# Kernel tuning notes

Hardware: AMD Instinct MI355X
Metric: run time of the kernel (lower is better)

The kernel has to match this reference:

```python
import jax, jax.numpy as jnp
import numpy as np

N_HEADS = 16
ROPE_THETA = 10000.0


def _rope_cos_sin(T, head_dim, dtype):
    # freqs: (head_dim//2,), angles: (T, head_dim//2)
    freqs = 1.0 / ROPE_THETA ** (jnp.arange(0, head_dim, 2, dtype=jnp.float32) / head_dim)
    ang = jnp.arange(T, dtype=jnp.float32)[:, None] * freqs[None, :]
    return jnp.cos(ang).astype(dtype), jnp.sin(ang).astype(dtype)


def _apply_rope(x, cos, sin):
    # x: (B, H, T, D); cos/sin: (T, D//2)
    D = x.shape[-1]
    x1, x2 = x[..., : D // 2], x[..., D // 2 :]
    return jnp.concatenate([x1 * cos - x2 * sin, x1 * sin + x2 * cos], axis=-1)


def setup_inputs() -> dict:
    key = jax.random.key(0)
    ks = jax.random.split(key, 5)
    B, T, C = 2, 2048, 1024
    x = jax.random.normal(ks[0], (B, T, C), dtype=jnp.float32)
    w_attn = jax.random.normal(ks[1], (C, 3 * C), dtype=jnp.float32) * (C ** -0.5)
    b_attn = jax.random.normal(ks[2], (3 * C,), dtype=jnp.float32) * 0.02
    w_proj = jax.random.normal(ks[3], (C, C), dtype=jnp.float32) * (C ** -0.5)
    b_proj = jax.random.normal(ks[4], (C,), dtype=jnp.float32) * 0.02
    return {
        "x": x,
        "w_attn": w_attn,
        "b_attn": b_attn,
        "w_proj": w_proj,
        "b_proj": b_proj,
        "last_k_no_attend": 0,
        "window_size": 0,
    }


def reference(x, w_attn, b_attn, w_proj, b_proj, last_k_no_attend, window_size):
    B, T, C = x.shape
    H = N_HEADS
    D = C // H
    qkv = x @ w_attn + b_attn  # (B, T, 3C)
    q, k, v = jnp.split(qkv, 3, axis=-1)
    # (B, T, C) -> (B, H, T, D)
    to_heads = lambda t: t.reshape(B, T, H, D).transpose(0, 2, 1, 3)
    q, k, v = to_heads(q), to_heads(k), to_heads(v)
    cos, sin = _rope_cos_sin(T, D, x.dtype)
    q = _apply_rope(q, cos, sin)
    k = _apply_rope(k, cos, sin)
    scale = D ** -0.5
    attn = jnp.einsum("bhqd,bhkd->bhqk", q, k) * scale  # (B, H, T, T)
    causal = jnp.tril(jnp.ones((T, T), dtype=bool))
    attn = jnp.where(causal, attn, -jnp.inf)
    # last_k_no_attend/window_size default to 0 -> the custom-mask branch is
    # skipped (the nonzero branch in the source is ill-defined: it zeroes
    # entire rows producing NaN softmax).
    attn = jax.nn.softmax(attn, axis=-1)
    y = jnp.einsum("bhqk,bhkd->bhqd", attn, v)  # (B, H, T, D)
    y = y.transpose(0, 2, 1, 3).reshape(B, T, C)
    return y @ w_proj + b_proj
```

## Files before the change

kernel.cpp:

```cpp
#include <hip/hip_runtime.h>
#include <hip/hip_bf16.h>

typedef __bf16 bf16_t;
typedef __bf16 bf16x8 __attribute__((ext_vector_type(8)));
typedef float f32x4 __attribute__((ext_vector_type(4)));
typedef float f32x8v __attribute__((ext_vector_type(8)));

#define B_    2
#define T_    2048
#define C_    1024
#define H_    16
#define D_    64
#define M_    4096
#define NQKV_ 3072
#define PLD   72
#define NQT2  16
#define GTILE (128 * 64)
#define SLOT2 32768
#define KSB   4096
#define VTB   (64 * PLD)

static __device__ __forceinline__ float  bf2f(bf16_t x) { return (float)x; }
static __device__ __forceinline__ bf16_t f2bf(float x)  { return (bf16_t)x; }

typedef const __attribute__((address_space(1))) void gas_void;
typedef __attribute__((address_space(3))) void las_void;
static __device__ __forceinline__ void gld16(const void* g, void* l) {
  __builtin_amdgcn_global_load_lds((gas_void*)g, (las_void*)l, 16, 0, 0);
}

__global__ __launch_bounds__(256) void rope_tab_k(float2* __restrict__ tab) {
  int i = blockIdx.x * 256 + threadIdx.x;
  int tpos = i >> 5, d = i & 31;
  float fr = exp2f(-(float)d * (13.287712379549449f / 32.0f));
  float ang = (float)tpos * fr;
  tab[i] = make_float2(cosf(ang), sinf(ang));
}

__global__ __launch_bounds__(256) void f32_to_bf16_k(const float* __restrict__ in,
                                                     bf16_t* __restrict__ out) {
  const int i = (blockIdx.x * 256 + threadIdx.x) * 8;
  f32x8v v = *(const f32x8v*)(in + i);
  bf16x8 h;
#pragma unroll
  for (int j = 0; j < 8; ++j) h[j] = f2bf(v[j]);
  *(bf16x8*)(out + i) = h;
}

__global__ __launch_bounds__(256) void transpose_f32_bf16(const float* __restrict__ in,
                                                          bf16_t* __restrict__ out,
                                                          int R, int Ccols) {
  __shared__ bf16_t tile[32][33];
  int tx = threadIdx.x & 31, ty = threadIdx.x >> 5;
  int c0 = blockIdx.x * 32, r0 = blockIdx.y * 32;
#pragma unroll
  for (int j = 0; j < 4; ++j)
    tile[ty + j * 8][tx] = f2bf(in[(size_t)(r0 + ty + j * 8) * Ccols + c0 + tx]);
  __syncthreads();
#pragma unroll
  for (int j = 0; j < 4; ++j)
    out[(size_t)(c0 + ty + j * 8) * R + r0 + tx] = tile[tx][ty + j * 8];
}

__device__ __forceinline__ void gemm_core(const bf16_t* __restrict__ A,
                                          const bf16_t* __restrict__ Bt,
                                          int m0, int n0,
                                          bf16_t* sm,
                                          f32x4 acc[4][4]) {
  const int t    = threadIdx.x;
  const int lane = t & 63, w = t >> 6;
  const int wr = (w >> 1) * 64, wc = (w & 1) * 64;
  const int l15 = lane & 15, g4 = lane >> 4;

  const f32x4 z4 = {0.f, 0.f, 0.f, 0.f};
#pragma unroll
  for (int i = 0; i < 4; ++i)
#pragma unroll
    for (int j = 0; j < 4; ++j) acc[i][j] = z4;

  const int srow = w * 32 + (lane >> 3);
  const int sel8 = (lane & 7) * 8;
  const bf16_t* gA = A  + (size_t)(m0 + srow) * C_ + sel8;
  const bf16_t* gB = Bt + (size_t)(n0 + srow) * C_ + sel8;
  const int dOff = (w * 32) * 64;

#pragma unroll
  for (int j = 0; j < 4; ++j) {
    gld16(gA + (size_t)(j * 8) * C_, sm + dOff + j * 8 * 64);
    gld16(gB + (size_t)(j * 8) * C_, sm + GTILE + dOff + j * 8 * 64);
  }
  __syncthreads();

  int cur = 0;
  for (int kt = 0; kt < C_ / 64; ++kt) {
    if (kt + 1 < C_ / 64) {
      const int k0 = (kt + 1) * 64;
      bf16_t* nA = sm + (cur ^ 1) * (2 * GTILE);
      bf16_t* nB = nA + GTILE;
#pragma unroll
      for (int j = 0; j < 4; ++j) {
        gld16(gA + (size_t)(j * 8) * C_ + k0, nA + dOff + j * 8 * 64);
        gld16(gB + (size_t)(j * 8) * C_ + k0, nB + dOff + j * 8 * 64);
      }
    }
    const bf16_t* lA = sm + cur * (2 * GTILE);
    const bf16_t* lB = lA + GTILE;
#pragma unroll
    for (int ks = 0; ks < 2; ++ks) {
      bf16x8 af[4], bfv[4];
#pragma unroll
      for (int mi = 0; mi < 4; ++mi)
        af[mi] = *(const bf16x8*)&lA[(wr + mi * 16 + l15) * 64 + ks * 32 + g4 * 8];
#pragma unroll
      for (int ni = 0; ni < 4; ++ni)
        bfv[ni] = *(const bf16x8*)&lB[(wc + ni * 16 + l15) * 64 + ks * 32 + g4 * 8];
#pragma unroll
      for (int mi = 0; mi < 4; ++mi)
#pragma unroll
        for (int ni = 0; ni < 4; ++ni)
          acc[mi][ni] = __builtin_amdgcn_mfma_f32_16x16x32_bf16(af[mi], bfv[ni],
                                                                acc[mi][ni], 0, 0, 0);
    }
    __syncthreads();
    cur ^= 1;
  }
}

__global__ __launch_bounds__(512, 2) void qkv_gemm(const bf16_t* __restrict__ x,
                                                   const bf16_t* __restrict__ wT,
                                                   const float* __restrict__ bias,
                                                   const float2* __restrict__ rtab,
                                                   bf16_t* __restrict__ qo,
                                                   bf16_t* __restrict__ ko,
                                                   bf16_t* __restrict__ vo) {
  __shared__ __align__(16) bf16_t sm[2 * SLOT2];
  const int t = threadIdx.x;
  const int lane = t & 63, w = t >> 6;
  const int l15 = lane & 15, g4 = lane >> 4;
  const int wr = (w >> 1) * 32, wc = (w & 1) * 192;

  const int bid = blockIdx.x;
  const int swz = (bid & 7) * 32 + (bid >> 3);
  const int m0 = (swz & 31) * 128, n0 = (swz >> 5) * 384;

  const f32x4 z4 = {0.f, 0.f, 0.f, 0.f};
  f32x4 acc[2][12];
#pragma unroll
  for (int i = 0; i < 2; ++i)
#pragma unroll
    for (int j = 0; j < 12; ++j) acc[i][j] = z4;

  const int sr8 = lane >> 3;
  const int swc = ((lane & 7) ^ ((lane >> 3) & 7)) * 8;
  const bf16_t* gA = x  + (size_t)(m0 + w * 16 + sr8) * C_ + swc;
  const bf16_t* gB = wT + (size_t)(n0 + w * 48 + sr8) * C_ + swc;

#define QKV_STAGE(h)                                                            \
  {                                                                             \
    bf16_t* sl = sm + ((h) & 1) * SLOT2;                                        \
    const size_t kofs = (size_t)(h) * 64;                                       \
    gld16(gA + kofs,            sl + (w * 16 +  0) * 64);                       \
    gld16(gA +  8 * C_ + kofs,  sl + (w * 16 +  8) * 64);                       \
    gld16(gB + kofs,            sl + 8192 + (w * 48 +  0) * 64);                \
    gld16(gB +  8 * C_ + kofs,  sl + 8192 + (w * 48 +  8) * 64);                \
    gld16(gB + 16 * C_ + kofs,  sl + 8192 + (w * 48 + 16) * 64);                \
    gld16(gB + 24 * C_ + kofs,  sl + 8192 + (w * 48 + 24) * 64);                \
    gld16(gB + 32 * C_ + kofs,  sl + 8192 + (w * 48 + 32) * 64);                \
    gld16(gB + 40 * C_ + kofs,  sl + 8192 + (w * 48 + 40) * 64);                \
  }

  QKV_STAGE(0);

  const int csw = l15 & 7;

  for (int h = 0; h < 16; ++h) {
    asm volatile("s_waitcnt vmcnt(0)" ::: "memory");
    __builtin_amdgcn_sched_barrier(0);
    __builtin_amdgcn_s_barrier();
    __builtin_amdgcn_sched_barrier(0);
    if (h + 1 < 16) QKV_STAGE(h + 1);

    const bf16_t* sl = sm + (h & 1) * SLOT2;
#pragma unroll
    for (int ks = 0; ks < 2; ++ks) {
      bf16x8 af[2], bfv[12];
#pragma unroll
      for (int mi = 0; mi < 2; ++mi)
        af[mi] = *(const bf16x8*)&sl[(wr + mi * 16 + l15) * 64 + (((ks * 4 + g4) ^ csw) * 8)];
#pragma unroll
      for (int ni = 0; ni < 12; ++ni)
        bfv[ni] = *(const bf16x8*)&sl[8192 + (wc + ni * 16 + l15) * 64 + (((ks * 4 + g4) ^ csw) * 8)];
#pragma unroll
      for (int mi = 0; mi < 2; ++mi)
#pragma unroll
        for (int ni = 0; ni < 12; ++ni)
          acc[mi][ni] = __builtin_amdgcn_mfma_f32_16x16x32_bf16(af[mi], bfv[ni],
                                                                acc[mi][ni], 0, 0, 0);
    }
  }
#undef QKV_STAGE

  __syncthreads();
  bf16_t* stg = sm + w * 6144;

#pragma unroll
  for (int cc = 0; cc < 3; ++cc) {
    const int ngc = n0 + (w & 1) * 192 + cc * 64;
    const int sel = ngc >> 10;
    if (sel < 2) {
      const float qs = (sel == 0) ? 0.125f * 1.4426950408889634f : 1.0f;
#pragma unroll
      for (int mi = 0; mi < 2; ++mi) {
#pragma unroll
        for (int nq = 0; nq < 2; ++nq) {
          const int d1 = nq * 16 + l15;
          const float b1 = bias[ngc + d1];
          const float b2 = bias[ngc + d1 + 32];
#pragma unroll
          for (int r = 0; r < 4; ++r) {
            const int lrow = mi * 16 + g4 * 4 + r;
            const int tpos = (m0 + wr + lrow) & (T_ - 1);
            const float2 cs = rtab[tpos * 32 + d1];
            const float x1 = acc[mi][cc * 4 + nq][r]     + b1;
            const float x2 = acc[mi][cc * 4 + nq + 2][r] + b2;
            stg[lrow * 192 + cc * 64 + d1]      = f2bf((x1 * cs.x - x2 * cs.y) * qs);
            stg[lrow * 192 + cc * 64 + d1 + 32] = f2bf((x1 * cs.y + x2 * cs.x) * qs);
          }
        }
      }
    } else {
#pragma unroll
      for (int mi = 0; mi < 2; ++mi)
#pragma unroll
        for (int nq = 0; nq < 4; ++nq) {
          const int d = nq * 16 + l15;
          const float b1 = bias[ngc + d];
#pragma unroll
          for (int r = 0; r < 4; ++r)
            stg[(mi * 16 + g4 * 4 + r) * 192 + cc * 64 + d] = f2bf(acc[mi][cc * 4 + nq][r] + b1);
        }
    }
  }

  const int a  = lane >> 3;
  const int b8 = (lane & 7) * 8;
#pragma unroll
  for (int cc = 0; cc < 3; ++cc) {
    const int ngc = n0 + (w & 1) * 192 + cc * 64;
    const int sel = ngc >> 10;
    const int hh  = (ngc & 1023) >> 6;
    bf16_t* outp = (sel == 0) ? qo : (sel == 1 ? ko : vo);
#pragma unroll
    for (int pp = 0; pp < 4; ++pp) {
      const int lrow = pp * 8 + a;
      const int row  = m0 + wr + lrow;
      const int tpos = row & (T_ - 1);
      const int bb   = row >> 11;
      uint4 val = *(const uint4*)&stg[lrow * 192 + cc * 64 + b8];
      *(uint4*)(outp + ((size_t)(bb * H_ + hh) * T_ + tpos) * D_ + b8) = val;
    }
  }
}

__global__ __launch_bounds__(512) void attn_fwd(const bf16_t* __restrict__ q,
                                                const bf16_t* __restrict__ k,
                                                const bf16_t* __restrict__ v,
                                                bf16_t* __restrict__ y) {
  __shared__ __align__(16) bf16_t Ks[2 * KSB];
  __shared__ __align__(16) bf16_t Vt[2 * VTB];
  const int t = threadIdx.x;
  const int lane = t & 63, w = t >> 6;
  const int l15 = lane & 15, g4 = lane >> 4;

  const int f   = blockIdx.x;
  const int idx = f & 255;
  const int bh  = idx & 31;
  const int p   = idx >> 5;
  const int qt  = (f >> 8) ? (15 - p) : p;
  const int qb  = qt * 128;
  const size_t hb = (size_t)bh * T_ * D_;

  const int qrow = qb + w * 16 + l15;
  bf16x8 qf[2];
  qf[0] = *(const bf16x8*)(q + hb + (size_t)qrow * D_ + g4 * 8);
  qf[1] = *(const bf16x8*)(q + hb + (size_t)qrow * D_ + 32 + g4 * 8);

  const f32x4 z4 = {0.f, 0.f, 0.f, 0.f};
  f32x4 o[4];
#pragma unroll
  for (int i = 0; i < 4; ++i) o[i] = z4;
  float mx = -1e30f, L = 0.f;

  const int skk = t >> 3;
  const int sd0 = (t & 7) * 8;
  const int u   = t & 7;
  const int ksw = sd0 ^ ((skk & 7) * 8);
  const int slot = ((skk >> 5) & 1) * 32 + ((skk >> 2) & 3) * 8 + ((skk >> 4) & 1) * 4 + (skk & 3);
  const int pos  = (((slot >> 3) ^ u) << 3) | (slot & 7);
  const int rowb = qb + w * 16 + g4 * 4;

  const int ntiles = 2 * qt + 2;

  {
    uint4 kv0 = *(const uint4*)(k + hb + (size_t)skk * D_ + sd0);
    uint4 vv0 = *(const uint4*)(v + hb + (size_t)skk * D_ + sd0);
    *(uint4*)&Ks[skk * 64 + ksw] = kv0;
    const bf16_t* vb = (const bf16_t*)&vv0;
#pragma unroll
    for (int i = 0; i < 8; ++i)
      Vt[(sd0 + i) * PLD + pos] = vb[i];
  }
  __syncthreads();

  uint4 kv, vv;
  for (int it = 0; it < ntiles; ++it) {
    const int kb  = it * 64;
    const int cur = it & 1;
    const bool last = (it == ntiles - 1);

    if (it + 1 < ntiles) {
      const size_t nb = hb + (size_t)(kb + 64 + skk) * D_ + sd0;
      kv = *(const uint4*)(k + nb);
      vv = *(const uint4*)(v + nb);
    }

    if (!(last && w < 4)) {
      const bf16_t* KsC = Ks + cur * KSB;
      const bf16_t* VtC = Vt + cur * VTB;

      f32x4 s[4];
#pragma unroll
      for (int c = 0; c < 4; ++c) s[c] = z4;
#pragma unroll
      for (int ks = 0; ks < 2; ++ks)
#pragma unroll
        for (int c = 0; c < 4; ++c) {
          const int kr = c * 16 + l15;
          bf16x8 kf = *(const bf16x8*)&KsC[kr * 64 + ((ks * 32 + g4 * 8) ^ ((kr & 7) * 8))];
          s[c] = __builtin_amdgcn_mfma_f32_16x16x32_bf16(kf, qf[ks], s[c], 0, 0, 0);
        }

      if (last || (it == ntiles - 2 && w < 4)) {
#pragma unroll
        for (int c = 0; c < 4; ++c)
#pragma unroll
          for (int r = 0; r < 4; ++r)
            if (kb + c * 16 + g4 * 4 + r > qrow) s[c][r] = -1e30f;
      }

      float tm = -1e30f;
#pragma unroll
      for (int c = 0; c < 4; ++c)
#pragma unroll
        for (int r = 0; r < 4; ++r) tm = fmaxf(tm, s[c][r]);
      tm = fmaxf(tm, __shfl_xor(tm, 16));
      tm = fmaxf(tm, __shfl_xor(tm, 32));
      if (!__all(tm - mx <= 8.0f)) {
        const float mnew = fmaxf(mx, tm);
        const float sc = exp2f(mx - mnew);
        L *= sc;
        float scr[4];
#pragma unroll
        for (int r = 0; r < 4; ++r)
          scr[r] = __shfl(sc, (lane & 48) | (g4 * 4 + r));
#pragma unroll
        for (int nf = 0; nf < 4; ++nf)
#pragma unroll
          for (int r = 0; r < 4; ++r) o[nf][r] *= scr[r];
        mx = mnew;
      }
      float rs = 0.f;
#pragma unroll
      for (int c = 0; c < 4; ++c)
#pragma unroll
        for (int r = 0; r < 4; ++r) {
          s[c][r] = exp2f(s[c][r] - mx);
          rs += s[c][r];
        }
      rs += __shfl_xor(rs, 16);
      rs += __shfl_xor(rs, 32);
      L += rs;

      bf16x8 ap0, ap1;
#pragma unroll
      for (int r = 0; r < 4; ++r) {
        ap0[r]     = f2bf(s[0][r]);
        ap0[4 + r] = f2bf(s[1][r]);
        ap1[r]     = f2bf(s[2][r]);
        ap1[4 + r] = f2bf(s[3][r]);
      }

#pragma unroll
      for (int nf = 0; nf < 4; ++nf) {
        const int d  = nf * 16 + l15;
        const int h3 = (2 * nf + (l15 >> 3)) & 7;
        bf16x8 vf0 = *(const bf16x8*)&VtC[d * PLD + ((g4 ^ h3) << 3)];
        bf16x8 vf1 = *(const bf16x8*)&VtC[d * PLD + (((g4 + 4) ^ h3) << 3)];
        o[nf] = __builtin_amdgcn_mfma_f32_16x16x32_bf16(ap0, vf0, o[nf], 0, 0, 0);
        o[nf] = __builtin_amdgcn_mfma_f32_16x16x32_bf16(ap1, vf1, o[nf], 0, 0, 0);
      }
    }

    if (it + 1 < ntiles) {
      bf16_t* KsN = Ks + (cur ^ 1) * KSB;
      bf16_t* VtN = Vt + (cur ^ 1) * VTB;
      *(uint4*)&KsN[skk * 64 + ksw] = kv;
      const bf16_t* vb = (const bf16_t*)&vv;
#pragma unroll
      for (int i = 0; i < 8; ++i)
        VtN[(sd0 + i) * PLD + pos] = vb[i];
    }
    __syncthreads();
  }

  const int bb = bh / H_, hh = bh % H_;
  float il[4];
#pragma unroll
  for (int r = 0; r < 4; ++r)
    il[r] = 1.0f / __shfl(L, (lane & 48) | (g4 * 4 + r));
#pragma unroll
  for (int nf = 0; nf < 4; ++nf)
#pragma unroll
    for (int r = 0; r < 4; ++r) {
      const int row = rowb + r;
      y[(size_t)(bb * T_ + row) * C_ + hh * D_ + nf * 16 + l15] = f2bf(o[nf][r] * il[r]);
    }
}

__global__ __launch_bounds__(256) void proj_gemm(const bf16_t* __restrict__ yin,
                                                 const bf16_t* __restrict__ wT,
                                                 const float* __restrict__ bias,
                                                 float* __restrict__ out) {
  __shared__ __align__(16) bf16_t smem[4 * GTILE];
  f32x4 acc[4][4];
  const int bid = blockIdx.x;
  const int swz = (bid & 7) * 32 + (bid >> 3);
  const int m0 = (swz & 31) * 128, n0 = (swz >> 5) * 128;
  gemm_core(yin, wT, m0, n0, smem, acc);

  const int t = threadIdx.x;
  const int lane = t & 63, w = t >> 6;
  const int wr = (w >> 1) * 64, wc = (w & 1) * 64;
  const int l15 = lane & 15, g4 = lane >> 4;
  const int ng = n0 + wc;
#pragma unroll
  for (int mi = 0; mi < 4; ++mi) {
    const int rowb = m0 + wr + mi * 16 + g4 * 4;
#pragma unroll
    for (int ni = 0; ni < 4; ++ni) {
      const int n = ng + ni * 16 + l15;
      const float b1 = bias[n];
#pragma unroll
      for (int r = 0; r < 4; ++r)
        out[(size_t)(rowb + r) * C_ + n] = acc[mi][ni][r] + b1;
    }
  }
}

extern "C" void kernel_launch(void* const* d_in, const int* in_sizes, int n_in,
                              void* d_out, int out_size, void* d_ws, size_t ws_size,
                              hipStream_t stream) {
  (void)in_sizes; (void)n_in; (void)out_size; (void)ws_size;
  const float* x      = (const float*)d_in[0];
  const float* w_attn = (const float*)d_in[1];
  const float* b_attn = (const float*)d_in[2];
  const float* w_proj = (const float*)d_in[3];
  const float* b_proj = (const float*)d_in[4];
  float* out = (float*)d_out;

  char* ws = (char*)d_ws;
  bf16_t* wTa = (bf16_t*)ws;  ws += (size_t)NQKV_ * C_ * 2;
  bf16_t* wTp = (bf16_t*)ws;  ws += (size_t)C_ * C_ * 2;
  bf16_t* qb  = (bf16_t*)ws;  ws += (size_t)B_ * H_ * T_ * D_ * 2;
  bf16_t* kb  = (bf16_t*)ws;  ws += (size_t)B_ * H_ * T_ * D_ * 2;
  bf16_t* vb  = (bf16_t*)ws;  ws += (size_t)B_ * H_ * T_ * D_ * 2;
  bf16_t* yb  = (bf16_t*)ws;  ws += (size_t)B_ * T_ * C_ * 2;
  float2* rtab = (float2*)ws; ws += (size_t)T_ * 32 * sizeof(float2);
  bf16_t* x_bf = yb;

  rope_tab_k<<<dim3(T_ * 32 / 256), 256, 0, stream>>>(rtab);
  transpose_f32_bf16<<<dim3(NQKV_ / 32, C_ / 32), 256, 0, stream>>>(w_attn, wTa, C_, NQKV_);
  transpose_f32_bf16<<<dim3(C_ / 32,   C_ / 32), 256, 0, stream>>>(w_proj, wTp, C_, C_);
  f32_to_bf16_k<<<dim3(M_ * C_ / (256 * 8)), 256, 0, stream>>>(x, x_bf);
  qkv_gemm<<<dim3((M_ / 128) * (NQKV_ / 384)), 512, 0, stream>>>(x_bf, wTa, b_attn, rtab, qb, kb, vb);
  attn_fwd<<<dim3(NQT2 * 32), 512, 0, stream>>>(qb, kb, vb, yb);
  proj_gemm<<<dim3((M_ / 128) * (C_ / 128)), 256, 0, stream>>>(yb, wTp, b_proj, out);
}
```

Before: 111.9 us.

## Software-pipeline attention so QK of next tile overlaps softmax/PV of previous

Restructures the attention loop into a one-stage software pipeline. The QK^T MFMAs for tile `it` are issued in the same iteration as the softmax and PV MFMAs for tile `it-1`, with an extra drain iteration at the end. V moves to triple buffering in LDS so the tile being consumed is not overwritten by the prefetch. The aim is to hide exp/reduction latency behind matrix-core work, at the cost of more registers (two score sets live at once) and extra LDS.

```diff
diff --git a/kernel.cpp b/kernel.cpp
--- a/kernel.cpp
+++ b/kernel.cpp
@@ -267,7 +267,7 @@
                                                 const bf16_t* __restrict__ v,
                                                 bf16_t* __restrict__ y) {
   __shared__ __align__(16) bf16_t Ks[2 * KSB];
-  __shared__ __align__(16) bf16_t Vt[2 * VTB];
+  __shared__ __align__(16) bf16_t Vt[3 * VTB];
   const int t = threadIdx.x;
   const int lane = t & 63, w = t >> 6;
   const int l15 = lane & 15, g4 = lane >> 4;
@@ -312,57 +312,59 @@
   }
   __syncthreads();
 
+  f32x4 sp[4];
+  bool prevValid = false;
+  int kread = 0, vwr = 1, vfin = 2;
   uint4 kv, vv;
-  for (int it = 0; it < ntiles; ++it) {
-    const int kb  = it * 64;
-    const int cur = it & 1;
-    const bool last = (it == ntiles - 1);
-
-    if (it + 1 < ntiles) {
-      const size_t nb = hb + (size_t)(kb + 64 + skk) * D_ + sd0;
+
+  for (int it = 0; it <= ntiles; ++it) {
+    const bool hasNext = (it + 1 < ntiles);
+    if (hasNext) {
+      const size_t nb = hb + (size_t)((it + 1) * 64 + skk) * D_ + sd0;
       kv = *(const uint4*)(k + nb);
       vv = *(const uint4*)(v + nb);
     }
 
-    if (!(last && w < 4)) {
-      const bf16_t* KsC = Ks + cur * KSB;
-      const bf16_t* VtC = Vt + cur * VTB;
-
-      f32x4 s[4];
-#pragma unroll
-      for (int c = 0; c < 4; ++c) s[c] = z4;
+    const bool doQK = (it < ntiles) && !((it == ntiles - 1) && w < 4);
+    f32x4 sc[4];
+    if (doQK) {
+      const int kb = it * 64;
+      const bf16_t* KsC = Ks + kread * KSB;
+#pragma unroll
+      for (int c = 0; c < 4; ++c) sc[c] = z4;
 #pragma unroll
       for (int ks = 0; ks < 2; ++ks)
 #pragma unroll
         for (int c = 0; c < 4; ++c) {
           const int kr = c * 16 + l15;
           bf16x8 kf = *(const bf16x8*)&KsC[kr * 64 + ((ks * 32 + g4 * 8) ^ ((kr & 7) * 8))];
-          s[c] = __builtin_amdgcn_mfma_f32_16x16x32_bf16(kf, qf[ks], s[c], 0, 0, 0);
+          sc[c] = __builtin_amdgcn_mfma_f32_16x16x32_bf16(kf, qf[ks], sc[c], 0, 0, 0);
         }
-
-      if (last || (it == ntiles - 2 && w < 4)) {
+      if (it == ntiles - 1 || (it == ntiles - 2 && w < 4)) {
 #pragma unroll
         for (int c = 0; c < 4; ++c)
 #pragma unroll
           for (int r = 0; r < 4; ++r)
-            if (kb + c * 16 + g4 * 4 + r > qrow) s[c][r] = -1e30f;
+            if (kb + c * 16 + g4 * 4 + r > qrow) sc[c][r] = -1e30f;
       }
-
+    }
+
+    if (prevValid) {
       float tm = -1e30f;
 #pragma unroll
       for (int c = 0; c < 4; ++c)
 #pragma unroll
-        for (int r = 0; r < 4; ++r) tm = fmaxf(tm, s[c][r]);
+        for (int r = 0; r < 4; ++r) tm = fmaxf(tm, sp[c][r]);
       tm = fmaxf(tm, __shfl_xor(tm, 16));
       tm = fmaxf(tm, __shfl_xor(tm, 32));
       if (!__all(tm - mx <= 8.0f)) {
         const float mnew = fmaxf(mx, tm);
-        const float sc = exp2f(mx - mnew);
-        L *= sc;
+        const float sc2 = exp2f(mx - mnew);
+        L *= sc2;
         float scr[4];
 #pragma unroll
         for (int r = 0; r < 4; ++r)
-          scr[r] = __shfl(sc, (lane & 48) | (g4 * 4 + r));
+          scr[r] = __shfl(sc2, (lane & 48) | (g4 * 4 + r));
 #pragma unroll
         for (int nf = 0; nf < 4; ++nf)
 #pragma unroll
@@ -374,8 +376,8 @@
       for (int c = 0; c < 4; ++c)
 #pragma unroll
         for (int r = 0; r < 4; ++r) {
-          s[c][r] = exp2f(s[c][r] - mx);
-          rs += s[c][r];
+          sp[c][r] = exp2f(sp[c][r] - mx);
+          rs += sp[c][r];
         }
       rs += __shfl_xor(rs, 16);
       rs += __shfl_xor(rs, 32);
@@ -384,12 +386,12 @@
       bf16x8 ap0, ap1;
 #pragma unroll
       for (int r = 0; r < 4; ++r) {
-        ap0[r]     = f2bf(s[0][r]);
-        ap0[4 + r] = f2bf(s[1][r]);
-        ap1[r]     = f2bf(s[2][r]);
-        ap1[4 + r] = f2bf(s[3][r]);
+        ap0[r]     = f2bf(sp[0][r]);
+        ap0[4 + r] = f2bf(sp[1][r]);
+        ap1[r]     = f2bf(sp[2][r]);
+        ap1[4 + r] = f2bf(sp[3][r]);
       }
-
+      const bf16_t* VtC = Vt + vfin * VTB;
 #pragma unroll
       for (int nf = 0; nf < 4; ++nf) {
         const int d  = nf * 16 + l15;
@@ -401,16 +403,26 @@
       }
     }
 
-    if (it + 1 < ntiles) {
-      bf16_t* KsN = Ks + (cur ^ 1) * KSB;
-      bf16_t* VtN = Vt + (cur ^ 1) * VTB;
+    if (doQK) {
+#pragma unroll
+      for (int c = 0; c < 4; ++c) sp[c] = sc[c];
+    }
+    prevValid = doQK;
+
+    if (hasNext) {
+      bf16_t* KsN = Ks + (kread ^ 1) * KSB;
+      bf16_t* VtN = Vt + vwr * VTB;
       *(uint4*)&KsN[skk * 64 + ksw] = kv;
       const bf16_t* vb = (const bf16_t*)&vv;
 #pragma unroll
       for (int i = 0; i < 8; ++i)
         VtN[(sd0 + i) * PLD + pos] = vb[i];
     }
-    __syncthreads();
+    if (it < ntiles) __syncthreads();
+
+    kread ^= 1;
+    vwr  = (vwr  == 2) ? 0 : vwr + 1;
+    vfin = (vfin == 2) ? 0 : vfin + 1;
   }
 
   const int bb = bh / H_, hh = bh % H_;
```

After: 113.5 us. About the same (+1.5%).
